# Performance work log

Hardware: AMD Instinct MI355X
Metric: run time of the kernel (lower is better)

## Reference

```python
import jax, jax.numpy as jnp
import numpy as np

N_HEAD = 16
MASK_SCALE = 10000.0  # matches torch buffer construction


def setup_inputs() -> dict:
    key = jax.random.key(0)
    k1, k2 = jax.random.split(key)
    B, T, C = 2, 2048, 1024
    x = jax.random.normal(k1, (B, T, C), dtype=jnp.float32)
    # packed q,k projection: nn.Linear(C, 2C, bias=False) -> weight [2C, C]
    W_attn = jax.random.normal(k2, (2 * C, C), dtype=jnp.float32) * 0.02
    alpha = jnp.array(1.0, dtype=jnp.float32)
    beta = jnp.array(0.1, dtype=jnp.float32)
    gamma = jnp.array(0.1, dtype=jnp.float32)
    return {"x": x, "W_attn": W_attn, "alpha": alpha, "beta": beta, "gamma": gamma}


def _shaped_attention(x, W_attn, alpha, beta, gamma):
    B, T, C = x.shape
    H = N_HEAD
    hd = C // H
    # packed projection then split into q, k (use_v=False -> v comes from x)
    qk = jnp.einsum('btc,oc->bto', x, W_attn)  # [B,T,2C]
    q, k = jnp.split(qk, 2, axis=-1)
    q = q.reshape(B, T, H, hd).transpose(0, 2, 1, 3)  # [B,H,T,hd]
    k = k.reshape(B, T, H, hd).transpose(0, 2, 1, 3)
    v = x.reshape(B, T, H, hd).transpose(0, 2, 1, 3)

    scores = jnp.einsum('bhqd,bhkd->bhqk', q, k) * (hd ** -0.5)
    tril = jnp.tril(jnp.ones((T, T), dtype=bool))
    scores = jnp.where(tril, scores, -jnp.inf)
    att = jax.nn.softmax(scores, axis=-1)  # [B,H,T,T]

    # fixed structured masks, built exactly as the torch buffers
    Id = jax.nn.softmax(jnp.eye(T, dtype=jnp.float32) * MASK_SCALE, axis=-1)
    MC = jax.nn.softmax(tril.astype(jnp.float32) * MASK_SCALE, axis=-1)

    shaped = beta * att + alpha * Id[None, None] - gamma * MC[None, None]
    y = jnp.einsum('bhqk,bhkd->bhqd', shaped, v)
    return y.transpose(0, 2, 1, 3).reshape(B, T, C)  # c_proj is Identity


def reference(x, W_attn, alpha, beta, gamma):
    return _shaped_attention(x, W_attn, alpha, beta, gamma)
```

## Files before the change

kernel.cpp:

```cpp
#include <hip/hip_runtime.h>
#include <hip/hip_bf16.h>

typedef __attribute__((ext_vector_type(8))) short bf16x8;
typedef __attribute__((ext_vector_type(4))) float f32x4;
typedef unsigned short u16;

#define B_  2
#define T_  2048
#define C_  1024
#define H_  16
#define HD_ 64

static __device__ __forceinline__ u16 f2bf(float f) {
  unsigned u = __float_as_uint(f);
  u += 0x7fffu + ((u >> 16) & 1u);
  return (u16)(u >> 16);
}

#define NW4 524288
__global__ __launch_bounds__(256) void prep(
    const float* __restrict__ X, const float* __restrict__ W,
    u16* __restrict__ Xb, u16* __restrict__ Wb,
    u16* __restrict__ Vf, float* __restrict__ SubP64)
{
  __shared__ u16 tr[64][65];
  __shared__ float cs[4][64];
  const int blk = blockIdx.x;
  const int tid = threadIdx.x;

  if (blk < 1024) {
    const int kt = blk & 31, bh = blk >> 5;
    const int b = bh >> 4, h = bh & 15;
    const int w = tid >> 6, lane = tid & 63;
    {
      const int row = tid >> 2;
      const int c0  = (tid & 3) * 16;
      const float* xp = X + ((size_t)b * T_ + kt * 64 + row) * C_ + h * 64 + c0;
      float vals[16];
#pragma unroll
      for (int q = 0; q < 4; ++q) {
        float4 v = *(const float4*)(xp + q * 4);
        vals[q * 4 + 0] = v.x; vals[q * 4 + 1] = v.y;
        vals[q * 4 + 2] = v.z; vals[q * 4 + 3] = v.w;
      }
      u16 xb[16];
#pragma unroll
      for (int i = 0; i < 16; ++i) xb[i] = f2bf(vals[i]);
      u16* xq = Xb + ((size_t)(b * T_ + kt * 64 + row)) * C_ + h * 64 + c0;
      *(bf16x8*)xq       = *(const bf16x8*)&xb[0];
      *(bf16x8*)(xq + 8) = *(const bf16x8*)&xb[8];
#pragma unroll
      for (int i = 0; i < 16; ++i) tr[row][c0 + i] = xb[i];
#pragma unroll
      for (int m = 4; m <= 32; m <<= 1)
#pragma unroll
        for (int i = 0; i < 16; ++i) vals[i] += __shfl_xor(vals[i], m);
      if (lane < 4) {
        float* dst = &cs[w][lane * 16];
#pragma unroll
        for (int q = 0; q < 4; ++q) {
          f32x4 s4 = { vals[q * 4 + 0], vals[q * 4 + 1], vals[q * 4 + 2], vals[q * 4 + 3] };
          *(f32x4*)&dst[q * 4] = s4;
        }
      }
    }
    __syncthreads();
    {
      const int w = tid >> 6, lane = tid & 63;
      const int quad = (lane >> 4), l16 = lane & 15;
      u16* outb = Vf + ((size_t)bh * 32 + kt) * 4096;
#pragma unroll
      for (int c = 0; c < 2; ++c) {
        u16 tmp[8];
#pragma unroll
        for (int j = 0; j < 8; ++j) tmp[j] = tr[c * 32 + quad * 8 + j][w * 16 + l16];
        *(bf16x8*)&outb[((w * 2 + c) * 64 + lane) * 8] = *(const bf16x8*)tmp;
      }
    }
    if (tid < 64)
      SubP64[(size_t)bh * 2048 + kt * 64 + tid] =
          cs[0][tid] + cs[1][tid] + cs[2][tid] + cs[3][tid];
  } else {
    int i = (blk - 1024) * 256 + tid;
    float4 v = ((const float4*)W)[i];
    ushort4 u = { f2bf(v.x), f2bf(v.y), f2bf(v.z), f2bf(v.w) };
    ((ushort4*)Wb)[i] = u;
  }
}

__global__ __launch_bounds__(256) void gemm_qk(
    const u16* __restrict__ Xb, const u16* __restrict__ Wb,
    u16* __restrict__ Qo, u16* __restrict__ Kf)
{
  __shared__ __align__(16) u16 As[2][128 * 64];
  __shared__ __align__(16) u16 Bs[2][128 * 64];

  const int tid  = threadIdx.x;
  const int w    = tid >> 6;
  const int lane = tid & 63;
  const int quad = lane >> 4;
  const int l16  = lane & 15;
  const int m0 = blockIdx.y * 128;
  const int n0 = blockIdx.x * 128;

  const int grow = w * 8 + ((lane >> 3) & 7);
  const int gcol = (lane & 7) * 8;

  f32x4 zero = {0.f, 0.f, 0.f, 0.f};
  f32x4 acc[4][4];
#pragma unroll
  for (int i = 0; i < 4; ++i)
#pragma unroll
    for (int j = 0; j < 4; ++j) acc[i][j] = zero;

  const int wr = (w >> 1) * 64, wc = (w & 1) * 64;

  const u16* gax = Xb + (size_t)(m0 + grow) * C_ + gcol;
  const u16* gbx = Wb + (size_t)(n0 + grow) * C_ + gcol;

#define GISSUE(K, BUF)                                                      \
  {                                                                         \
    _Pragma("unroll") for (int r = 0; r < 4; ++r) {                         \
      __builtin_amdgcn_global_load_lds(                                     \
          (const __attribute__((address_space(1))) void*)(gax + (size_t)r * 32 * C_ + (K)), \
          (__attribute__((address_space(3))) void*)&As[BUF][(w * 8 + r * 32) * 64], \
          16, 0, 0);                                                        \
      __builtin_amdgcn_global_load_lds(                                     \
          (const __attribute__((address_space(1))) void*)(gbx + (size_t)r * 32 * C_ + (K)), \
          (__attribute__((address_space(3))) void*)&Bs[BUF][(w * 8 + r * 32) * 64], \
          16, 0, 0);                                                        \
    }                                                                       \
  }

  GISSUE(0, 0);
#pragma unroll 2
  for (int it = 0; it < 16; ++it) {
    const int cur = it & 1;
    __syncthreads();
    if (it < 15) GISSUE((it + 1) * 64, cur ^ 1);
#pragma unroll
    for (int c = 0; c < 2; ++c) {
      bf16x8 af[4], bf[4];
#pragma unroll
      for (int i = 0; i < 4; ++i)
        af[i] = *(const bf16x8*)&As[cur][(wr + i * 16 + l16) * 64 + c * 32 + quad * 8];
#pragma unroll
      for (int j = 0; j < 4; ++j)
        bf[j] = *(const bf16x8*)&Bs[cur][(wc + j * 16 + l16) * 64 + c * 32 + quad * 8];
#pragma unroll
      for (int i = 0; i < 4; ++i)
#pragma unroll
        for (int j = 0; j < 4; ++j)
          acc[i][j] = __builtin_amdgcn_mfma_f32_16x16x32_bf16(af[i], bf[j], acc[i][j], 0, 0, 0);
    }
  }
#undef GISSUE

#pragma unroll
  for (int i = 0; i < 4; ++i) {
    const int t_base = m0 + wr + i * 16;
    const int bidx = t_base >> 11;
    const int kt   = (t_base & 2047) >> 6;
    const int trow = (t_base & 2047) + quad * 4;
#pragma unroll
    for (int j = 0; j < 4; ++j) {
      const int n = n0 + wc + j * 16 + l16;
      if (n < C_) {
        const int hq = n >> 6, d = n & 63;
        u16* qp = Qo + (((size_t)bidx * H_ + hq) * T_ + trow) * HD_ + d;
#pragma unroll
        for (int r = 0; r < 4; ++r) qp[(size_t)r * HD_] = f2bf(0.125f * acc[i][j][r]);
      } else {
        const int nh = n - C_;
        const int hh = nh >> 6, d = nh & 63;
        u16* kp = Kf + (((((size_t)(bidx * H_ + hh) * 32 + kt) * 4 + i) * 2 + (d >> 5)) * 64
                        + ((d >> 3) & 3) * 16 + quad * 4) * 8 + (d & 7);
#pragma unroll
        for (int r = 0; r < 4; ++r) kp[(size_t)r * 8] = f2bf(acc[i][j][r]);
      }
    }
  }
}

__global__ __launch_bounds__(512) void attn_kernel(
    const u16* __restrict__ Q, const u16* __restrict__ Kf, const u16* __restrict__ Vf,
    const float* __restrict__ SubP64, const float* __restrict__ X, float* __restrict__ out,
    const float* __restrict__ alphap, const float* __restrict__ betap,
    const float* __restrict__ gammap)
{
  __shared__ __align__(16) char smem[51200];
  u16 (*Ks)[4096] = (u16(*)[4096])(smem);
  u16 (*Vs)[4096] = (u16(*)[4096])(smem + 16384);

  const int tid  = threadIdx.x;
  const int w    = tid >> 6;
  const int lane = tid & 63;
  const int quad = lane >> 4;
  const int l16  = lane & 15;
  const int jq = 15 - blockIdx.y;
  const int bh = blockIdx.x;
  const int b = bh >> 4, h = bh & 15;

  const int qt_w  = 2 * jq + (w >> 2);
  const int qtmax = 2 * jq + 1;
  const int mt    = (w & 3) * 16 + quad * 4;

  const u16* kfb = Kf + (size_t)bh * T_ * HD_;
  const u16* vfb = Vf + (size_t)bh * T_ * HD_;
  u16* pb = (u16*)(smem + 32768) + (size_t)w * 1152;

  bf16x8 qfrag[2];
  {
    const u16* qp = Q + ((size_t)bh * T_ + jq * 128 + w * 16 + l16) * HD_ + quad * 8;
    qfrag[0] = *(const bf16x8*)qp;
    qfrag[1] = *(const bf16x8*)(qp + 32);
  }

  bf16x8 onesf;
#pragma unroll
  for (int j = 0; j < 8; ++j) onesf[j] = (short)0x3F80;

  f32x4 zero = {0.f, 0.f, 0.f, 0.f};
  f32x4 acc[4] = {zero, zero, zero, zero};
  f32x4 accl = zero;

#define STAGE(KT, BUF)                                                        \
  {                                                                           \
    const u16* sb = (w < 4) ? kfb : vfb;                                      \
    u16* db = (w < 4) ? &Ks[BUF][0] : &Vs[BUF][0];                            \
    const int ch = (w & 3) * 2;                                               \
    _Pragma("unroll") for (int ci = 0; ci < 2; ++ci) {                        \
      __builtin_amdgcn_global_load_lds(                                       \
          (const __attribute__((address_space(1))) void*)(                    \
              sb + (size_t)(KT) * 4096 + (ch + ci) * 512 + lane * 8),         \
          (__attribute__((address_space(3))) void*)(db + (ch + ci) * 512),    \
          16, 0, 0);                                                          \
    }                                                                         \
  }

  STAGE(0, 0);
  for (int kt = 0; kt <= qtmax; ++kt) {
    const int cur = kt & 1;
    __syncthreads();
    if (kt < qtmax) STAGE(kt + 1, cur ^ 1);
    if (kt <= qt_w) {
      const u16* Ksb = Ks[cur];
      const u16* Vsb = Vs[cur];
      const bool diag = (kt == qt_w);

      f32x4 sfr[4] = {zero, zero, zero, zero};
#pragma unroll
      for (int cc = 0; cc < 2; ++cc)
#pragma unroll
        for (int nb = 0; nb < 4; ++nb) {
          bf16x8 kf = *(const bf16x8*)&Ksb[((nb * 2 + cc) * 64 + lane) * 8];
          sfr[nb] = __builtin_amdgcn_mfma_f32_16x16x32_bf16(qfrag[cc], kf, sfr[nb], 0, 0, 0);
        }

#pragma unroll
      for (int nb = 0; nb < 4; ++nb)
#pragma unroll
        for (int r = 0; r < 4; ++r) {
          float p = __expf(sfr[nb][r]);
          if (diag && (nb * 16 + l16 > mt + r)) p = 0.f;
          pb[(quad * 4 + r) * 72 + nb * 16 + l16] = f2bf(p);
        }

#pragma unroll
      for (int cc = 0; cc < 2; ++cc) {
        bf16x8 pk = *(const bf16x8*)&pb[l16 * 72 + cc * 32 + quad * 8];
        accl = __builtin_amdgcn_mfma_f32_16x16x32_bf16(pk, onesf, accl, 0, 0, 0);
#pragma unroll
        for (int nb = 0; nb < 4; ++nb) {
          bf16x8 vf = *(const bf16x8*)&Vsb[((nb * 2 + cc) * 64 + lane) * 8];
          acc[nb] = __builtin_amdgcn_mfma_f32_16x16x32_bf16(pk, vf, acc[nb], 0, 0, 0);
        }
      }
    }
  }
#undef STAGE

  __syncthreads();
  float* Xt = (float*)smem;
  float* G  = (float*)(smem + 34816);
  float* GP = (float*)(smem + 36864);

  {
    const int row = tid >> 2, c0 = (tid & 3) * 16;
    const float* xp = X + ((size_t)b * T_ + jq * 128 + row) * C_ + h * 64 + c0;
#pragma unroll
    for (int q = 0; q < 4; ++q) {
      float4 v = *(const float4*)(xp + q * 4);
      Xt[row * 68 + c0 + q * 4 + 0] = v.x;
      Xt[row * 68 + c0 + q * 4 + 1] = v.y;
      Xt[row * 68 + c0 + q * 4 + 2] = v.z;
      Xt[row * 68 + c0 + q * 4 + 3] = v.w;
    }
  }
  {
    float p = 0.f;
    for (int i = w; i < 2 * jq; i += 8)
      p += SubP64[(size_t)bh * 2048 + i * 64 + lane];
    GP[w * 64 + lane] = p;
  }
  __syncthreads();
  {
    float g = 0.f;
#pragma unroll
    for (int i = 0; i < 16; ++i) g += Xt[(w * 16 + i) * 68 + lane];
    G[w * 64 + lane] = g;
  }
  __syncthreads();
  {
    const float alpha = *alphap, gamma = *gammap;
    float run = 0.f;
#pragma unroll
    for (int k = 0; k < 8; ++k) run += GP[k * 64 + lane];
    for (int g = 0; g < w; ++g) run += G[g * 64 + lane];
    const int tbase = jq * 128 + w * 16;
#pragma unroll
    for (int i = 0; i < 16; ++i) {
      float v = Xt[(w * 16 + i) * 68 + lane];
      run += v;
      Xt[(w * 16 + i) * 68 + lane] =
          alpha * v - gamma * run * __builtin_amdgcn_rcpf((float)(tbase + i + 1));
    }
  }
  __syncthreads();

  {
    const float beta = *betap;
    float rl[4];
#pragma unroll
    for (int r = 0; r < 4; ++r) rl[r] = beta * __builtin_amdgcn_rcpf(accl[r]);
    const int myrow = w * 16 + quad * 4;
#pragma unroll
    for (int nb = 0; nb < 4; ++nb) {
#pragma unroll
      for (int r = 0; r < 4; ++r) {
        int t = jq * 128 + myrow + r;
        int d = nb * 16 + l16;
        out[((size_t)b * T_ + t) * C_ + h * 64 + d] =
            Xt[(myrow + r) * 68 + d] + rl[r] * acc[nb][r];
      }
    }
  }
}

extern "C" void kernel_launch(void* const* d_in, const int* in_sizes, int n_in,
                              void* d_out, int out_size, void* d_ws, size_t ws_size,
                              hipStream_t stream) {
  const float* x      = (const float*)d_in[0];
  const float* W_attn = (const float*)d_in[1];
  const float* alphap = (const float*)d_in[2];
  const float* betap  = (const float*)d_in[3];
  const float* gammap = (const float*)d_in[4];
  float* out = (float*)d_out;

  char* ws = (char*)d_ws;
  u16*   Qb     = (u16*)(ws);
  u16*   Kfb    = (u16*)(ws + (8ull  << 20));
  u16*   Vfb    = (u16*)(ws + (16ull << 20));
  float* SubP64 = (float*)(ws + (24ull << 20));
  u16*   Xb     = (u16*)(ws + (25ull << 20));
  u16*   Wb     = (u16*)(ws + (33ull << 20));

  prep<<<3072, 256, 0, stream>>>(x, W_attn, Xb, Wb, Vfb, SubP64);
  gemm_qk<<<dim3(16, 32), 256, 0, stream>>>(Xb, Wb, Qb, Kfb);
  attn_kernel<<<dim3(32, 16), 512, 0, stream>>>(Qb, Kfb, Vfb, SubP64, x, out,
                                                alphap, betap, gammap);
}
```

Measured before the change: 150.4 us.

## Split KV tiles across wave halves and keep P in registers via permlane swaps

```diff
diff --git a/kernel.cpp b/kernel.cpp
--- a/kernel.cpp
+++ b/kernel.cpp
@@ -3,6 +3,7 @@
 
 typedef __attribute__((ext_vector_type(8))) short bf16x8;
 typedef __attribute__((ext_vector_type(4))) float f32x4;
+typedef __attribute__((ext_vector_type(2))) unsigned int u32x2;
 typedef unsigned short u16;
 
 #define B_  2
@@ -66,7 +67,6 @@
     }
     __syncthreads();
     {
-      const int w = tid >> 6, lane = tid & 63;
       const int quad = (lane >> 4), l16 = lane & 15;
       u16* outb = Vf + ((size_t)bh * 32 + kt) * 4096;
 #pragma unroll
@@ -188,30 +188,27 @@
     const float* __restrict__ alphap, const float* __restrict__ betap,
     const float* __restrict__ gammap)
 {
-  __shared__ __align__(16) char smem[51200];
+  __shared__ __align__(16) char smem[32768];
   u16 (*Ks)[4096] = (u16(*)[4096])(smem);
   u16 (*Vs)[4096] = (u16(*)[4096])(smem + 16384);
 
   const int tid  = threadIdx.x;
   const int w    = tid >> 6;
+  const int wq   = w & 3;
+  const int parity = w >> 2;
   const int lane = tid & 63;
   const int quad = lane >> 4;
   const int l16  = lane & 15;
-  const int jq = 15 - blockIdx.y;
+  const int qt = 31 - blockIdx.y;
   const int bh = blockIdx.x;
   const int b = bh >> 4, h = bh & 15;
 
-  const int qt_w  = 2 * jq + (w >> 2);
-  const int qtmax = 2 * jq + 1;
-  const int mt    = (w & 3) * 16 + quad * 4;
-
   const u16* kfb = Kf + (size_t)bh * T_ * HD_;
   const u16* vfb = Vf + (size_t)bh * T_ * HD_;
-  u16* pb = (u16*)(smem + 32768) + (size_t)w * 1152;
 
   bf16x8 qfrag[2];
   {
-    const u16* qp = Q + ((size_t)bh * T_ + jq * 128 + w * 16 + l16) * HD_ + quad * 8;
+    const u16* qp = Q + ((size_t)bh * T_ + qt * 64 + wq * 16 + l16) * HD_ + quad * 8;
     qfrag[0] = *(const bf16x8*)qp;
     qfrag[1] = *(const bf16x8*)(qp + 32);
   }
@@ -239,57 +236,87 @@
   }
 
   STAGE(0, 0);
-  for (int kt = 0; kt <= qtmax; ++kt) {
+  for (int kt = 0; kt <= qt; ++kt) {
     const int cur = kt & 1;
     __syncthreads();
-    if (kt < qtmax) STAGE(kt + 1, cur ^ 1);
-    if (kt <= qt_w) {
-      const u16* Ksb = Ks[cur];
-      const u16* Vsb = Vs[cur];
-      const bool diag = (kt == qt_w);
-
-      f32x4 sfr[4] = {zero, zero, zero, zero};
-#pragma unroll
-      for (int cc = 0; cc < 2; ++cc)
-#pragma unroll
-        for (int nb = 0; nb < 4; ++nb) {
-          bf16x8 kf = *(const bf16x8*)&Ksb[((nb * 2 + cc) * 64 + lane) * 8];
-          sfr[nb] = __builtin_amdgcn_mfma_f32_16x16x32_bf16(qfrag[cc], kf, sfr[nb], 0, 0, 0);
-        }
-
-#pragma unroll
-      for (int nb = 0; nb < 4; ++nb)
-#pragma unroll
-        for (int r = 0; r < 4; ++r) {
-          float p = __expf(sfr[nb][r]);
-          if (diag && (nb * 16 + l16 > mt + r)) p = 0.f;
-          pb[(quad * 4 + r) * 72 + nb * 16 + l16] = f2bf(p);
-        }
-
-#pragma unroll
-      for (int cc = 0; cc < 2; ++cc) {
-        bf16x8 pk = *(const bf16x8*)&pb[l16 * 72 + cc * 32 + quad * 8];
-        accl = __builtin_amdgcn_mfma_f32_16x16x32_bf16(pk, onesf, accl, 0, 0, 0);
-#pragma unroll
-        for (int nb = 0; nb < 4; ++nb) {
-          bf16x8 vf = *(const bf16x8*)&Vsb[((nb * 2 + cc) * 64 + lane) * 8];
-          acc[nb] = __builtin_amdgcn_mfma_f32_16x16x32_bf16(pk, vf, acc[nb], 0, 0, 0);
-        }
+    if (kt < qt) STAGE(kt + 1, cur ^ 1);
+    if (cur != parity) continue;
+    const u16* Ksb = Ks[cur];
+    const u16* Vsb = Vs[cur];
+    const bool diag = (kt == qt);
+
+    f32x4 sfr[4] = {zero, zero, zero, zero};
+#pragma unroll
+    for (int cc = 0; cc < 2; ++cc)
+#pragma unroll
+      for (int nb = 0; nb < 4; ++nb) {
+        bf16x8 kf = *(const bf16x8*)&Ksb[((nb * 2 + cc) * 64 + lane) * 8];
+        sfr[nb] = __builtin_amdgcn_mfma_f32_16x16x32_bf16(kf, qfrag[cc], sfr[nb], 0, 0, 0);
+      }
+
+    unsigned pkk[4][2];
+#pragma unroll
+    for (int nb = 0; nb < 4; ++nb) {
+      float p[4];
+#pragma unroll
+      for (int r = 0; r < 4; ++r) {
+        float e = __expf(sfr[nb][r]);
+        if (diag && (nb * 16 + quad * 4 + r > wq * 16 + l16)) e = 0.f;
+        p[r] = e;
+      }
+      asm("v_cvt_pk_bf16_f32 %0, %1, %2" : "=v"(pkk[nb][0]) : "v"(p[0]), "v"(p[1]));
+      asm("v_cvt_pk_bf16_f32 %0, %1, %2" : "=v"(pkk[nb][1]) : "v"(p[2]), "v"(p[3]));
+    }
+
+#pragma unroll
+    for (int g = 0; g < 2; ++g) {
+      u32x2 s0 = __builtin_amdgcn_permlane32_swap(pkk[2 * g][0], pkk[2 * g + 1][0], false, false);
+      u32x2 s1 = __builtin_amdgcn_permlane32_swap(pkk[2 * g][1], pkk[2 * g + 1][1], false, false);
+      u32x2 t0 = __builtin_amdgcn_permlane16_swap(s0[0], s0[1], false, false);
+      u32x2 t1 = __builtin_amdgcn_permlane16_swap(s1[0], s1[1], false, false);
+      union { unsigned u[4]; bf16x8 v; } pa;
+      pa.u[0] = t0[0]; pa.u[1] = t1[0]; pa.u[2] = t0[1]; pa.u[3] = t1[1];
+      accl = __builtin_amdgcn_mfma_f32_16x16x32_bf16(pa.v, onesf, accl, 0, 0, 0);
+#pragma unroll
+      for (int nb = 0; nb < 4; ++nb) {
+        bf16x8 vf = *(const bf16x8*)&Vsb[((nb * 2 + g) * 64 + lane) * 8];
+        acc[nb] = __builtin_amdgcn_mfma_f32_16x16x32_bf16(pa.v, vf, acc[nb], 0, 0, 0);
       }
     }
   }
 #undef STAGE
 
   __syncthreads();
+  {
+    float* comb = (float*)smem;
+    if (parity == 1) {
+      float* dst = comb + ((size_t)(wq * 64 + lane)) * 20;
+#pragma unroll
+      for (int nb = 0; nb < 4; ++nb) *(f32x4*)&dst[nb * 4] = acc[nb];
+      *(f32x4*)&dst[16] = accl;
+    }
+    __syncthreads();
+    if (parity == 0) {
+      const float* src = comb + ((size_t)(wq * 64 + lane)) * 20;
+#pragma unroll
+      for (int nb = 0; nb < 4; ++nb) {
+        f32x4 t = *(const f32x4*)&src[nb * 4];
+        acc[nb] += t;
+      }
+      accl += *(const f32x4*)&src[16];
+    }
+  }
+  __syncthreads();
+
   float* Xt = (float*)smem;
-  float* G  = (float*)(smem + 34816);
-  float* GP = (float*)(smem + 36864);
-
-  {
-    const int row = tid >> 2, c0 = (tid & 3) * 16;
-    const float* xp = X + ((size_t)b * T_ + jq * 128 + row) * C_ + h * 64 + c0;
-#pragma unroll
-    for (int q = 0; q < 4; ++q) {
+  float* G  = (float*)(smem + 17408);
+  float* GP = (float*)(smem + 19456);
+
+  {
+    const int row = tid >> 3, c0 = (tid & 7) * 8;
+    const float* xp = X + ((size_t)b * T_ + qt * 64 + row) * C_ + h * 64 + c0;
+#pragma unroll
+    for (int q = 0; q < 2; ++q) {
       float4 v = *(const float4*)(xp + q * 4);
       Xt[row * 68 + c0 + q * 4 + 0] = v.x;
       Xt[row * 68 + c0 + q * 4 + 1] = v.y;
@@ -299,7 +326,7 @@
   }
   {
     float p = 0.f;
-    for (int i = w; i < 2 * jq; i += 8)
+    for (int i = w; i < qt; i += 8)
       p += SubP64[(size_t)bh * 2048 + i * 64 + lane];
     GP[w * 64 + lane] = p;
   }
@@ -307,7 +334,7 @@
   {
     float g = 0.f;
 #pragma unroll
-    for (int i = 0; i < 16; ++i) g += Xt[(w * 16 + i) * 68 + lane];
+    for (int i = 0; i < 8; ++i) g += Xt[(w * 8 + i) * 68 + lane];
     G[w * 64 + lane] = g;
   }
   __syncthreads();
@@ -317,28 +344,28 @@
 #pragma unroll
     for (int k = 0; k < 8; ++k) run += GP[k * 64 + lane];
     for (int g = 0; g < w; ++g) run += G[g * 64 + lane];
-    const int tbase = jq * 128 + w * 16;
-#pragma unroll
-    for (int i = 0; i < 16; ++i) {
-      float v = Xt[(w * 16 + i) * 68 + lane];
+    const int tbase = qt * 64 + w * 8;
+#pragma unroll
+    for (int i = 0; i < 8; ++i) {
+      float v = Xt[(w * 8 + i) * 68 + lane];
       run += v;
-      Xt[(w * 16 + i) * 68 + lane] =
+      Xt[(w * 8 + i) * 68 + lane] =
           alpha * v - gamma * run * __builtin_amdgcn_rcpf((float)(tbase + i + 1));
     }
   }
   __syncthreads();
 
-  {
+  if (parity == 0) {
     const float beta = *betap;
     float rl[4];
 #pragma unroll
     for (int r = 0; r < 4; ++r) rl[r] = beta * __builtin_amdgcn_rcpf(accl[r]);
-    const int myrow = w * 16 + quad * 4;
+    const int myrow = wq * 16 + quad * 4;
 #pragma unroll
     for (int nb = 0; nb < 4; ++nb) {
 #pragma unroll
       for (int r = 0; r < 4; ++r) {
-        int t = jq * 128 + myrow + r;
+        int t = qt * 64 + myrow + r;
         int d = nb * 16 + l16;
         out[((size_t)b * T_ + t) * C_ + h * 64 + d] =
             Xt[(myrow + r) * 68 + d] + rl[r] * acc[nb][r];
@@ -367,6 +394,6 @@
 
   prep<<<3072, 256, 0, stream>>>(x, W_attn, Xb, Wb, Vfb, SubP64);
   gemm_qk<<<dim3(16, 32), 256, 0, stream>>>(Xb, Wb, Qb, Kfb);
-  attn_kernel<<<dim3(32, 16), 512, 0, stream>>>(Qb, Kfb, Vfb, SubP64, x, out,
+  attn_kernel<<<dim3(32, 32), 512, 0, stream>>>(Qb, Kfb, Vfb, SubP64, x, out,
                                                 alphap, betap, gammap);
 }
```

New measurement: 140.0 us. 6.9% less time.

## Keep attention probabilities in registers via permlane swaps and swizzle GEMM LDS tiles

Applied to the files above, without the earlier changes.

```diff
diff --git a/kernel.cpp b/kernel.cpp
--- a/kernel.cpp
+++ b/kernel.cpp
@@ -3,6 +3,7 @@
 
 typedef __attribute__((ext_vector_type(8))) short bf16x8;
 typedef __attribute__((ext_vector_type(4))) float f32x4;
+typedef __attribute__((ext_vector_type(2))) unsigned int u32x2;
 typedef unsigned short u16;
 
 #define B_  2
@@ -66,7 +67,6 @@
     }
     __syncthreads();
     {
-      const int w = tid >> 6, lane = tid & 63;
       const int quad = (lane >> 4), l16 = lane & 15;
       u16* outb = Vf + ((size_t)bh * 32 + kt) * 4096;
 #pragma unroll
@@ -104,7 +104,7 @@
   const int n0 = blockIdx.x * 128;
 
   const int grow = w * 8 + ((lane >> 3) & 7);
-  const int gcol = (lane & 7) * 8;
+  const int gcol = (((lane & 7) ^ ((lane >> 3) & 7)) * 8);
 
   f32x4 zero = {0.f, 0.f, 0.f, 0.f};
   f32x4 acc[4][4];
@@ -143,10 +143,12 @@
       bf16x8 af[4], bf[4];
 #pragma unroll
       for (int i = 0; i < 4; ++i)
-        af[i] = *(const bf16x8*)&As[cur][(wr + i * 16 + l16) * 64 + c * 32 + quad * 8];
+        af[i] = *(const bf16x8*)&As[cur][(wr + i * 16 + l16) * 64
+                                         + (((c * 4 + quad) ^ (l16 & 7)) * 8)];
 #pragma unroll
       for (int j = 0; j < 4; ++j)
-        bf[j] = *(const bf16x8*)&Bs[cur][(wc + j * 16 + l16) * 64 + c * 32 + quad * 8];
+        bf[j] = *(const bf16x8*)&Bs[cur][(wc + j * 16 + l16) * 64
+                                         + (((c * 4 + quad) ^ (l16 & 7)) * 8)];
 #pragma unroll
       for (int i = 0; i < 4; ++i)
 #pragma unroll
@@ -188,12 +190,13 @@
     const float* __restrict__ alphap, const float* __restrict__ betap,
     const float* __restrict__ gammap)
 {
-  __shared__ __align__(16) char smem[51200];
+  __shared__ __align__(16) char smem[38912];
   u16 (*Ks)[4096] = (u16(*)[4096])(smem);
   u16 (*Vs)[4096] = (u16(*)[4096])(smem + 16384);
 
   const int tid  = threadIdx.x;
   const int w    = tid >> 6;
+  const int wq   = w & 3;
   const int lane = tid & 63;
   const int quad = lane >> 4;
   const int l16  = lane & 15;
@@ -203,11 +206,9 @@
 
   const int qt_w  = 2 * jq + (w >> 2);
   const int qtmax = 2 * jq + 1;
-  const int mt    = (w & 3) * 16 + quad * 4;
 
   const u16* kfb = Kf + (size_t)bh * T_ * HD_;
   const u16* vfb = Vf + (size_t)bh * T_ * HD_;
-  u16* pb = (u16*)(smem + 32768) + (size_t)w * 1152;
 
   bf16x8 qfrag[2];
   {
@@ -254,26 +255,36 @@
 #pragma unroll
         for (int nb = 0; nb < 4; ++nb) {
           bf16x8 kf = *(const bf16x8*)&Ksb[((nb * 2 + cc) * 64 + lane) * 8];
-          sfr[nb] = __builtin_amdgcn_mfma_f32_16x16x32_bf16(qfrag[cc], kf, sfr[nb], 0, 0, 0);
+          sfr[nb] = __builtin_amdgcn_mfma_f32_16x16x32_bf16(kf, qfrag[cc], sfr[nb], 0, 0, 0);
         }
 
-#pragma unroll
-      for (int nb = 0; nb < 4; ++nb)
+      unsigned pkk[4][2];
+#pragma unroll
+      for (int nb = 0; nb < 4; ++nb) {
+        float p[4];
 #pragma unroll
         for (int r = 0; r < 4; ++r) {
-          float p = __expf(sfr[nb][r]);
-          if (diag && (nb * 16 + l16 > mt + r)) p = 0.f;
-          pb[(quad * 4 + r) * 72 + nb * 16 + l16] = f2bf(p);
+          float e = __expf(sfr[nb][r]);
+          if (diag && (nb * 16 + quad * 4 + r > wq * 16 + l16)) e = 0.f;
+          p[r] = e;
         }
-
-#pragma unroll
-      for (int cc = 0; cc < 2; ++cc) {
-        bf16x8 pk = *(const bf16x8*)&pb[l16 * 72 + cc * 32 + quad * 8];
-        accl = __builtin_amdgcn_mfma_f32_16x16x32_bf16(pk, onesf, accl, 0, 0, 0);
+        asm("v_cvt_pk_bf16_f32 %0, %1, %2" : "=v"(pkk[nb][0]) : "v"(p[0]), "v"(p[1]));
+        asm("v_cvt_pk_bf16_f32 %0, %1, %2" : "=v"(pkk[nb][1]) : "v"(p[2]), "v"(p[3]));
+      }
+
+#pragma unroll
+      for (int g = 0; g < 2; ++g) {
+        u32x2 s0 = __builtin_amdgcn_permlane32_swap(pkk[2 * g][0], pkk[2 * g + 1][0], false, false);
+        u32x2 s1 = __builtin_amdgcn_permlane32_swap(pkk[2 * g][1], pkk[2 * g + 1][1], false, false);
+        u32x2 t0 = __builtin_amdgcn_permlane16_swap(s0[0], s0[1], false, false);
+        u32x2 t1 = __builtin_amdgcn_permlane16_swap(s1[0], s1[1], false, false);
+        union { unsigned u[4]; bf16x8 v; } pa;
+        pa.u[0] = t0[0]; pa.u[1] = t1[0]; pa.u[2] = t0[1]; pa.u[3] = t1[1];
+        accl = __builtin_amdgcn_mfma_f32_16x16x32_bf16(pa.v, onesf, accl, 0, 0, 0);
 #pragma unroll
         for (int nb = 0; nb < 4; ++nb) {
-          bf16x8 vf = *(const bf16x8*)&Vsb[((nb * 2 + cc) * 64 + lane) * 8];
-          acc[nb] = __builtin_amdgcn_mfma_f32_16x16x32_bf16(pk, vf, acc[nb], 0, 0, 0);
+          bf16x8 vf = *(const bf16x8*)&Vsb[((nb * 2 + g) * 64 + lane) * 8];
+          acc[nb] = __builtin_amdgcn_mfma_f32_16x16x32_bf16(pa.v, vf, acc[nb], 0, 0, 0);
         }
       }
     }
```

Result: faster. 143.7 us (-4.4%).
